# Performance work log

Hardware: AMD Instinct MI355X
Metric: run time of the kernel (lower is better)

Reference implementation:

```python
import jax, jax.numpy as jnp
import numpy as np

KE = 14.3996
ALPHA = 0.3
CUTOFF = 10.0
K_MAX = 6
N_ATOMS = 100000
N_PAIRS = 6400000
N_MOL = 64


def _generate_kvecs():
    kr = np.arange(0, K_MAX + 1, dtype=np.float32)
    kr = np.concatenate([kr, -kr[1:]])
    # cartesian product of (kr, kr, kr)
    g = np.stack(np.meshgrid(kr, kr, kr, indexing='ij'), axis=-1).reshape(-1, 3)
    norm = (g ** 2).sum(axis=1)
    mask = (norm <= K_MAX ** 2 + 2) & (norm != 0)
    return jnp.asarray(g[mask])  # [1020, 3]


def setup_inputs() -> dict:
    key = jax.random.key(0)
    k1, k2, k3, k4, k5, k6, k7 = jax.random.split(key, 7)
    partial_charges = jax.random.normal(k1, (N_ATOMS, 1), dtype=jnp.float32)
    # pair displacement vectors; scale so typical |r_ij| ~ 3-6 A, avoids d ~ 0
    Rij = jax.random.normal(k2, (N_PAIRS, 3), dtype=jnp.float32) * 3.0 + 1.0
    R = jax.random.uniform(k3, (N_ATOMS, 3), dtype=jnp.float32) * 20.0
    # orthorhombic-ish invertible cells: diag(~20) + small perturbation
    cell = jnp.eye(3, dtype=jnp.float32)[None] * 20.0 \
        + jax.random.uniform(k4, (N_MOL, 3, 3), dtype=jnp.float32) * 0.1
    idx_m = jnp.sort(jax.random.randint(k5, (N_ATOMS,), 0, N_MOL)).astype(jnp.int64)
    idx_i = jax.random.randint(k6, (N_PAIRS,), 0, N_ATOMS).astype(jnp.int64)
    idx_j = jax.random.randint(k7, (N_PAIRS,), 0, N_ATOMS).astype(jnp.int64)
    kvecs = _generate_kvecs()
    return {"partial_charges": partial_charges, "Rij": Rij, "R": R, "cell": cell,
            "kvecs": kvecs, "idx_m": idx_m, "idx_i": idx_i, "idx_j": idx_j}


def reference(partial_charges, Rij, R, cell, kvecs, idx_m, idx_i, idx_j):
    q = partial_charges.squeeze(-1)                      # [A]
    d_ij = jnp.linalg.norm(Rij, axis=1)                  # [P]
    sqrt_a = jnp.sqrt(jnp.float32(ALPHA))

    # ---- real space: gather q, erfc-screened pair potential, double scatter ----
    f_r = jax.scipy.special.erfc(sqrt_a * d_ij) / d_ij
    f_r_cut = jax.scipy.special.erfc(sqrt_a * CUTOFF) / CUTOFF
    pot_ij = q[idx_i] * q[idx_j] * (f_r - f_r_cut)
    pot_ij = jnp.where(d_ij <= CUTOFF, pot_ij, jnp.zeros_like(pot_ij))
    y_atom = jax.ops.segment_sum(pot_ij, idx_i, num_segments=N_ATOMS)
    y_real = 0.5 * KE * jax.ops.segment_sum(y_atom, idx_m, num_segments=N_MOL)

    # ---- reciprocal space ----
    two_pi = 2.0 * jnp.float32(np.pi)
    recip_box = two_pi * jnp.transpose(jnp.linalg.inv(cell), (0, 2, 1))  # [M,3,3]
    v_box = jnp.abs(jnp.linalg.det(cell))                                # [M]
    prefactor = two_pi / v_box
    kv = jnp.einsum('kd,mde->mke', kvecs, recip_box)     # [M,K,3]
    k_sq = jnp.sum(kv ** 2, axis=2)                      # [M,K]
    q_gauss = jnp.exp(-0.25 * k_sq / ALPHA)              # [M,K]
    # per-atom phase: gather per-molecule k-vectors, dot with positions
    kdp = jnp.einsum('akd,ad->ak', kv[idx_m], R)         # [A,K]
    q_real = jax.ops.segment_sum(q[:, None] * jnp.cos(kdp), idx_m, num_segments=N_MOL)
    q_imag = jax.ops.segment_sum(q[:, None] * jnp.sin(kdp), idx_m, num_segments=N_MOL)
    q_dens = q_real ** 2 + q_imag ** 2                   # [M,K]
    y_ewald = prefactor * jnp.sum(q_dens * q_gauss / k_sq, axis=1)
    self_int = jnp.sqrt(ALPHA / np.pi) * jax.ops.segment_sum(q ** 2, idx_m, num_segments=N_MOL)
    y_recip = KE * (y_ewald - self_int)

    return y_real + y_recip                              # [M]
```

## Files before the change

kernel.cpp:

```cpp
#include <hip/hip_runtime.h>
#include <math.h>

#define KE_C     14.3996f
#define ALPHA_C  0.3f
#define CUTOFF_C 10.0f
#define TWO_PI_C 6.283185307179586f
#define ASPL     32
#define NK2      512
#define NREAL    2048

typedef float vfloat4 __attribute__((ext_vector_type(4)));
typedef int   vint4   __attribute__((ext_vector_type(4)));

__device__ __forceinline__ void sincos_rev(float x, float* s, float* c) {
    float f = __builtin_amdgcn_fractf(x);
    *s = __builtin_amdgcn_sinf(f);
    *c = __builtin_amdgcn_cosf(f);
}

__device__ __forceinline__ float inv3x3(const float* c, float* inv) {
    float a00 = c[0], a01 = c[1], a02 = c[2];
    float a10 = c[3], a11 = c[4], a12 = c[5];
    float a20 = c[6], a21 = c[7], a22 = c[8];
    float det = a00 * (a11 * a22 - a12 * a21)
              - a01 * (a10 * a22 - a12 * a20)
              + a02 * (a10 * a21 - a11 * a20);
    float id = 1.0f / det;
    inv[0] = (a11 * a22 - a12 * a21) * id;
    inv[1] = (a02 * a21 - a01 * a22) * id;
    inv[2] = (a01 * a12 - a02 * a11) * id;
    inv[3] = (a12 * a20 - a10 * a22) * id;
    inv[4] = (a00 * a22 - a02 * a20) * id;
    inv[5] = (a02 * a10 - a00 * a12) * id;
    inv[6] = (a10 * a21 - a11 * a20) * id;
    inv[7] = (a01 * a20 - a00 * a21) * id;
    inv[8] = (a00 * a11 - a01 * a10) * id;
    return det;
}

__global__ __launch_bounds__(256) void k_setup(const float* __restrict__ R,
                                               const float* __restrict__ q,
                                               const int* __restrict__ idx_m,
                                               const float* __restrict__ cell,
                                               const float* __restrict__ kvecs,
                                               float4* __restrict__ S4,
                                               float2* __restrict__ QM,
                                               float* __restrict__ SI,
                                               int* __restrict__ bounds,
                                               float4* __restrict__ KH,
                                               int* __restrict__ cnt,
                                               int natoms, int nmol, int nk, int NA) {
    int bid = blockIdx.x;
    int tid = threadIdx.x;
    if (bid < NA) {
        __shared__ float si[64];
        if (tid < 64) si[tid] = 0.0f;
        __syncthreads();
        int a = bid * 256 + tid;
        if (a < natoms) {
            int m = idx_m[a];
            float inv[9];
            inv3x3(cell + m * 9, inv);
            float r0 = R[3 * a], r1 = R[3 * a + 1], r2 = R[3 * a + 2];
            float s0 = inv[0] * r0 + inv[3] * r1 + inv[6] * r2;
            float s1 = inv[1] * r0 + inv[4] * r1 + inv[7] * r2;
            float s2 = inv[2] * r0 + inv[5] * r1 + inv[8] * r2;
            float qa = q[a];
            S4[a] = make_float4(s0, s1, s2, qa);
            QM[a] = make_float2(qa, __int_as_float(m));
            atomicAdd(&si[m & 63], qa * qa);
        }
        __syncthreads();
        if (tid < 64) atomicAdd(&SI[tid], si[tid]);
    } else if (bid == NA) {
        int m = tid;
        if (m <= nmol) {
            int lo = 0, hi = natoms;
            while (lo < hi) {
                int mid = (lo + hi) >> 1;
                if (idx_m[mid] < m) lo = mid + 1; else hi = mid;
            }
            bounds[m] = lo;
        }
    } else {
        for (int k = tid; k < nk; k += 256) {
            float gx = kvecs[3 * k], gy = kvecs[3 * k + 1], gz = kvecs[3 * k + 2];
            bool pos = (gx > 0.5f) ||
                       (fabsf(gx) < 0.5f && (gy > 0.5f ||
                        (fabsf(gy) < 0.5f && gz > 0.5f)));
            if (pos) {
                int s = atomicAdd(cnt, 1);
                KH[s] = make_float4(gx, gy, gz, 0.0f);
            }
        }
    }
}

__global__ __launch_bounds__(256) void k_recip(const float4* __restrict__ S4,
                                               const float4* __restrict__ KH,
                                               const int* __restrict__ bounds,
                                               float* __restrict__ QR,
                                               float* __restrict__ QI) {
    int tid = threadIdx.x;
    int bid = blockIdx.x;
    int m  = bid / ASPL;
    int ac = bid % ASPL;
    int s0 = bounds[m], s1 = bounds[m + 1];
    int per = (s1 - s0 + ASPL - 1) / ASPL;
    int a0 = s0 + ac * per;
    int a1 = min(a0 + per, s1);
    float4 g0 = KH[tid];
    float4 g1 = KH[tid + 256];
    float qr0 = 0.f, qi0 = 0.f, qr1 = 0.f, qi1 = 0.f;
#pragma unroll 4
    for (int t = a0; t < a1; ++t) {
        float4 s = S4[t];
        float ph0 = fmaf(g0.x, s.x, fmaf(g0.y, s.y, g0.z * s.z));
        float ph1 = fmaf(g1.x, s.x, fmaf(g1.y, s.y, g1.z * s.z));
        float sn0, cs0, sn1, cs1;
        sincos_rev(ph0, &sn0, &cs0);
        sincos_rev(ph1, &sn1, &cs1);
        qr0 = fmaf(s.w, cs0, qr0);
        qi0 = fmaf(s.w, sn0, qi0);
        qr1 = fmaf(s.w, cs1, qr1);
        qi1 = fmaf(s.w, sn1, qi1);
    }
    atomicAdd(&QR[m * NK2 + tid], qr0);
    atomicAdd(&QI[m * NK2 + tid], qi0);
    atomicAdd(&QR[m * NK2 + tid + 256], qr1);
    atomicAdd(&QI[m * NK2 + tid + 256], qi1);
}

__global__ __launch_bounds__(256, 8) void k_real(const float* __restrict__ Rij,
                                                 const int* __restrict__ idx_i,
                                                 const int* __restrict__ idx_j,
                                                 const float2* __restrict__ QM,
                                                 float* __restrict__ YRpad, int npairs) {
    __shared__ float acc[4][64];
    int tid = threadIdx.x;
    int wave = tid >> 6;
    acc[wave][tid & 63] = 0.0f;
    __syncthreads();
    const float sqa = 0.5477225575051661f;
    const float frcut = erfcf(sqa * CUTOFF_C) / CUTOFF_C;
    int nchunk = npairs >> 2;
    int stride = NREAL * 256;
    for (int c = blockIdx.x * 256 + tid; c < nchunk; c += stride) {
        int p = c << 2;
        vint4 ii = *(const vint4*)(idx_i + p);
        vint4 jj = *(const vint4*)(idx_j + p);
        const vfloat4* r4 = (const vfloat4*)(Rij + 3 * p);
        vfloat4 ra = r4[0], rb = r4[1], rc = r4[2];
        float x0 = ra.x, y0 = ra.y, z0 = ra.z;
        float x1 = ra.w, y1 = rb.x, z1 = rb.y;
        float x2 = rb.z, y2 = rb.w, z2 = rc.x;
        float x3 = rc.y, y3 = rc.z, z3 = rc.w;
        float2 qi0 = QM[ii.x], qi1 = QM[ii.y], qi2 = QM[ii.z], qi3 = QM[ii.w];
        float2 qj0 = QM[jj.x], qj1 = QM[jj.y], qj2 = QM[jj.z], qj3 = QM[jj.w];
        float d0 = sqrtf(x0 * x0 + y0 * y0 + z0 * z0);
        float d1 = sqrtf(x1 * x1 + y1 * y1 + z1 * z1);
        float d2 = sqrtf(x2 * x2 + y2 * y2 + z2 * z2);
        float d3 = sqrtf(x3 * x3 + y3 * y3 + z3 * z3);
        if (d0 <= CUTOFF_C)
            atomicAdd(&acc[wave][__float_as_int(qi0.y) & 63],
                      qi0.x * qj0.x * (erfcf(sqa * d0) / d0 - frcut));
        if (d1 <= CUTOFF_C)
            atomicAdd(&acc[wave][__float_as_int(qi1.y) & 63],
                      qi1.x * qj1.x * (erfcf(sqa * d1) / d1 - frcut));
        if (d2 <= CUTOFF_C)
            atomicAdd(&acc[wave][__float_as_int(qi2.y) & 63],
                      qi2.x * qj2.x * (erfcf(sqa * d2) / d2 - frcut));
        if (d3 <= CUTOFF_C)
            atomicAdd(&acc[wave][__float_as_int(qi3.y) & 63],
                      qi3.x * qj3.x * (erfcf(sqa * d3) / d3 - frcut));
    }
    if (blockIdx.x == 0 && tid == 0) {
        for (int p = (npairs >> 2) << 2; p < npairs; ++p) {
            float x = Rij[3 * p], y = Rij[3 * p + 1], z = Rij[3 * p + 2];
            float d = sqrtf(x * x + y * y + z * z);
            if (d <= CUTOFF_C) {
                float2 qi = QM[idx_i[p]];
                float2 qj = QM[idx_j[p]];
                atomicAdd(&acc[0][__float_as_int(qi.y) & 63],
                          qi.x * qj.x * (erfcf(sqa * d) / d - frcut));
            }
        }
    }
    __syncthreads();
    if (tid < 64) {
        float v = acc[0][tid] + acc[1][tid] + acc[2][tid] + acc[3][tid];
        atomicAdd(&YRpad[tid * 16], v);
    }
}

__global__ __launch_bounds__(256) void k_final(const float4* __restrict__ KH,
                                               const int* __restrict__ cnt,
                                               const float* __restrict__ cell,
                                               const float* __restrict__ QR,
                                               const float* __restrict__ QI,
                                               const float* __restrict__ YRpad,
                                               const float* __restrict__ SI,
                                               float* __restrict__ out) {
    int m = blockIdx.x;
    int tid = threadIdx.x;
    __shared__ float wsum[4];
    float inv[9];
    float det = inv3x3(cell + m * 9, inv);
    int nhalf = cnt[0];
    float acc = 0.0f;
    for (int k = tid; k < nhalf; k += 256) {
        float4 g = KH[k];
        float kv0 = TWO_PI_C * (g.x * inv[0] + g.y * inv[1] + g.z * inv[2]);
        float kv1 = TWO_PI_C * (g.x * inv[3] + g.y * inv[4] + g.z * inv[5]);
        float kv2 = TWO_PI_C * (g.x * inv[6] + g.y * inv[7] + g.z * inv[8]);
        float ksq = kv0 * kv0 + kv1 * kv1 + kv2 * kv2;
        float qr = QR[m * NK2 + k], qi = QI[m * NK2 + k];
        acc += (qr * qr + qi * qi) * __expf(-0.25f / ALPHA_C * ksq) / ksq;
    }
#pragma unroll
    for (int off = 32; off > 0; off >>= 1) acc += __shfl_down(acc, off, 64);
    if ((tid & 63) == 0) wsum[tid >> 6] = acc;
    __syncthreads();
    if (tid == 0) {
        float s = 2.0f * (wsum[0] + wsum[1] + wsum[2] + wsum[3]);
        float pref = TWO_PI_C / fabsf(det);
        float self_c = sqrtf(ALPHA_C / 3.14159265358979323846f);
        out[m] = 0.5f * KE_C * YRpad[m * 16] + KE_C * (pref * s - self_c * SI[m]);
    }
}

extern "C" void kernel_launch(void* const* d_in, const int* in_sizes, int n_in,
                              void* d_out, int out_size, void* d_ws, size_t ws_size,
                              hipStream_t stream) {
    const float* q     = (const float*)d_in[0];
    const float* Rij   = (const float*)d_in[1];
    const float* R     = (const float*)d_in[2];
    const float* cell  = (const float*)d_in[3];
    const float* kvecs = (const float*)d_in[4];
    const int*   idx_m = (const int*)d_in[5];
    const int*   idx_i = (const int*)d_in[6];
    const int*   idx_j = (const int*)d_in[7];

    int natoms = in_sizes[0];
    int npairs = in_sizes[1] / 3;
    int nmol   = in_sizes[3] / 9;
    int nk     = in_sizes[4] / 3;
    float* out = (float*)d_out;

    float*  W      = (float*)d_ws;
    int*    bounds = (int*)W;
    float4* S4     = (float4*)(W + 80);
    float2* QM     = (float2*)(W + 80 + 4 * (size_t)natoms);
    size_t  zoff   = 80 + 6 * (size_t)natoms;
    zoff = (zoff + 3) & ~(size_t)3;
    float4* KH     = (float4*)(W + zoff);
    float*  QR     = W + zoff + 4 * NK2;
    float*  QI     = QR + (size_t)nmol * NK2;
    float*  SI     = QI + (size_t)nmol * NK2;
    float*  YRpad  = SI + 64;
    int*    cnt    = (int*)(YRpad + 64 * 16);
    size_t zero_bytes = (4 * NK2 + (size_t)2 * nmol * NK2 + 64 + 64 * 16 + 4) * sizeof(float);
    (void)hipMemsetAsync(KH, 0, zero_bytes, stream);

    int NA = (natoms + 255) / 256;
    k_setup<<<NA + 2, 256, 0, stream>>>(R, q, idx_m, cell, kvecs, S4, QM, SI,
                                        bounds, KH, cnt, natoms, nmol, nk, NA);
    k_recip<<<nmol * ASPL, 256, 0, stream>>>(S4, KH, bounds, QR, QI);
    k_real <<<NREAL, 256, 0, stream>>>(Rij, idx_i, idx_j, QM, YRpad, npairs);
    k_final<<<nmol, 256, 0, stream>>>(KH, cnt, cell, QR, QI, YRpad, SI, out);
}
```

Measured before the change: 240.6 us.

## Bin real-space pairs by atom blocks so charge gathers hit LDS

Replaces the single real-space pair kernel with two passes. The first pass computes the screened pair potential, groups pairs into buckets keyed by the 4096-atom blocks of i and j, and writes compact (value, packed local indices) records. The second pass loads both blocks' charges into shared memory and accumulates the per-molecule sums from there. Charge and molecule id are packed into one word by stealing low mantissa bits, which costs a little precision. The change also adds extra global write and read traffic, a fixed per-bucket capacity that silently drops pairs on overflow, and a dependency on workspace size to enable the path.

```diff
diff --git a/kernel.cpp b/kernel.cpp
--- a/kernel.cpp
+++ b/kernel.cpp
@@ -8,6 +8,14 @@
 #define ASPL     32
 #define NK2      512
 #define NREAL    2048
+
+#define SHB      12
+#define NSL      25
+#define NBKT     (NSL * NSL)
+#define CAP      11264
+#define PA_BLOCKS 1024
+#define PA_TILE   1024
+#define CCHUNK    2
 
 typedef float vfloat4 __attribute__((ext_vector_type(4)));
 typedef int   vint4   __attribute__((ext_vector_type(4)));
@@ -45,6 +53,7 @@
                                                const float* __restrict__ kvecs,
                                                float4* __restrict__ S4,
                                                float2* __restrict__ QM,
+                                               unsigned int* __restrict__ QP,
                                                float* __restrict__ SI,
                                                int* __restrict__ bounds,
                                                float4* __restrict__ KH,
@@ -68,6 +77,7 @@
             float qa = q[a];
             S4[a] = make_float4(s0, s1, s2, qa);
             QM[a] = make_float2(qa, __int_as_float(m));
+            QP[a] = (__float_as_uint(qa) & ~63u) | (unsigned int)(m & 63);
             atomicAdd(&si[m & 63], qa * qa);
         }
         __syncthreads();
@@ -129,6 +139,116 @@
     atomicAdd(&QI[m * NK2 + tid], qi0);
     atomicAdd(&QR[m * NK2 + tid + 256], qr1);
     atomicAdd(&QI[m * NK2 + tid + 256], qi1);
+}
+
+__global__ __launch_bounds__(256) void k_binA(const float* __restrict__ Rij,
+                                              const int* __restrict__ idx_i,
+                                              const int* __restrict__ idx_j,
+                                              float2* __restrict__ Bkt,
+                                              int* __restrict__ gcnt, int npairs) {
+    __shared__ int h[NBKT];
+    __shared__ int pos[NBKT];
+    int tid = threadIdx.x;
+    const float sqa = 0.5477225575051661f;
+    const float frcut = erfcf(sqa * CUTOFF_C) / CUTOFF_C;
+    for (int base = blockIdx.x * PA_TILE; base < npairs; base += PA_BLOCKS * PA_TILE) {
+        for (int t = tid; t < NBKT; t += 256) h[t] = 0;
+        __syncthreads();
+        int p = base + tid * 4;
+        float fk[4];
+        int bk[4] = {-1, -1, -1, -1};
+        unsigned int pkk[4];
+#define DOPAIR(k, xx, yy, zz, iv, jv)                                         \
+        {                                                                     \
+            float d2_ = fmaf(xx, xx, fmaf(yy, yy, (zz) * (zz)));              \
+            float d_ = sqrtf(d2_);                                            \
+            if (d_ <= CUTOFF_C) {                                             \
+                fk[k] = erfcf(sqa * d_) / d_ - frcut;                         \
+                bk[k] = ((iv) >> SHB) * NSL + ((jv) >> SHB);                  \
+                pkk[k] = (unsigned int)(((iv) & 4095) | (((jv) & 4095) << SHB)); \
+            }                                                                 \
+        }
+        if (p + 4 <= npairs) {
+            vint4 ii = *(const vint4*)(idx_i + p);
+            vint4 jj = *(const vint4*)(idx_j + p);
+            const vfloat4* r4 = (const vfloat4*)(Rij + 3 * p);
+            vfloat4 ra = r4[0], rb = r4[1], rc = r4[2];
+            DOPAIR(0, ra.x, ra.y, ra.z, ii.x, jj.x)
+            DOPAIR(1, ra.w, rb.x, rb.y, ii.y, jj.y)
+            DOPAIR(2, rb.z, rb.w, rc.x, ii.z, jj.z)
+            DOPAIR(3, rc.y, rc.z, rc.w, ii.w, jj.w)
+        } else {
+#pragma unroll
+            for (int k = 0; k < 4; ++k) {
+                int pp = p + k;
+                if (pp < npairs) {
+                    float x = Rij[3 * pp], y = Rij[3 * pp + 1], z = Rij[3 * pp + 2];
+                    int iv = idx_i[pp], jv = idx_j[pp];
+                    DOPAIR(k, x, y, z, iv, jv)
+                }
+            }
+        }
+#undef DOPAIR
+#pragma unroll
+        for (int k = 0; k < 4; ++k)
+            if (bk[k] >= 0) atomicAdd(&h[bk[k]], 1);
+        __syncthreads();
+        for (int t = tid; t < NBKT; t += 256) {
+            int c = h[t];
+            pos[t] = c ? atomicAdd(&gcnt[t], c) : 0;
+        }
+        __syncthreads();
+#pragma unroll
+        for (int k = 0; k < 4; ++k)
+            if (bk[k] >= 0) {
+                int g = atomicAdd(&pos[bk[k]], 1);
+                if (g < CAP)
+                    Bkt[(size_t)bk[k] * CAP + g] = make_float2(fk[k], __uint_as_float(pkk[k]));
+            }
+        __syncthreads();
+    }
+}
+
+__global__ __launch_bounds__(256) void k_binB(const float2* __restrict__ Bkt,
+                                              const int* __restrict__ gcnt,
+                                              const unsigned int* __restrict__ QP,
+                                              float* __restrict__ YRpad, int natoms) {
+    __shared__ unsigned int Qi[4096];
+    __shared__ unsigned int Qj[4096];
+    __shared__ float acc[4][64];
+    int tid = threadIdx.x;
+    int wave = tid >> 6;
+    int b = blockIdx.x / CCHUNK;
+    int part = blockIdx.x % CCHUNK;
+    int si = b / NSL, sj = b % NSL;
+    int bi = si << SHB, bj = sj << SHB;
+    for (int t = tid; t < 4096; t += 256) {
+        int ai = bi + t;
+        Qi[t] = (ai < natoms) ? QP[ai] : 0u;
+        int aj = bj + t;
+        Qj[t] = (aj < natoms) ? QP[aj] : 0u;
+    }
+    acc[wave][tid & 63] = 0.0f;
+    __syncthreads();
+    int n = min(gcnt[b], CAP);
+    int lo = (n * part) / CCHUNK;
+    int hi = (n * (part + 1)) / CCHUNK;
+    const float2* src = Bkt + (size_t)b * CAP;
+    for (int r = lo + tid; r < hi; r += 256) {
+        float2 rec = src[r];
+        unsigned int pk = __float_as_uint(rec.y);
+        unsigned int il = pk & 4095u;
+        unsigned int jl = (pk >> SHB) & 4095u;
+        unsigned int up = Qi[il];
+        float qi = __uint_as_float(up & ~63u);
+        float qj = __uint_as_float(Qj[jl] & ~63u);
+        atomicAdd(&acc[wave][up & 63u], qi * qj * rec.x);
+    }
+    __syncthreads();
+    if (tid < 64) {
+        float v = acc[0][tid] + acc[1][tid] + acc[2][tid] + acc[3][tid];
+        if (v != 0.0f) atomicAdd(&YRpad[tid * 16], v);
+    }
 }
 
 __global__ __launch_bounds__(256, 8) void k_real(const float* __restrict__ Rij,
@@ -251,7 +371,8 @@
     int*    bounds = (int*)W;
     float4* S4     = (float4*)(W + 80);
     float2* QM     = (float2*)(W + 80 + 4 * (size_t)natoms);
-    size_t  zoff   = 80 + 6 * (size_t)natoms;
+    unsigned int* QP = (unsigned int*)(W + 80 + 6 * (size_t)natoms);
+    size_t  zoff   = 80 + 7 * (size_t)natoms;
     zoff = (zoff + 3) & ~(size_t)3;
     float4* KH     = (float4*)(W + zoff);
     float*  QR     = W + zoff + 4 * NK2;
@@ -259,13 +380,26 @@
     float*  SI     = QI + (size_t)nmol * NK2;
     float*  YRpad  = SI + 64;
     int*    cnt    = (int*)(YRpad + 64 * 16);
-    size_t zero_bytes = (4 * NK2 + (size_t)2 * nmol * NK2 + 64 + 64 * 16 + 4) * sizeof(float);
+    int*    gcnt   = cnt + 4;
+    size_t  boff   = (size_t)(gcnt + NBKT - (int*)W);
+    boff = (boff + 3) & ~(size_t)3;
+    float2* Bkt    = (float2*)(W + boff);
+    size_t  need   = (boff + 2 * (size_t)NBKT * CAP) * sizeof(float);
+    bool use_bin = (ws_size >= need);
+
+    size_t zero_bytes = (4 * NK2 + (size_t)2 * nmol * NK2 + 64 + 64 * 16 + 4 + NBKT) * sizeof(float);
     (void)hipMemsetAsync(KH, 0, zero_bytes, stream);
 
     int NA = (natoms + 255) / 256;
-    k_setup<<<NA + 2, 256, 0, stream>>>(R, q, idx_m, cell, kvecs, S4, QM, SI,
+    k_setup<<<NA + 2, 256, 0, stream>>>(R, q, idx_m, cell, kvecs, S4, QM, QP, SI,
                                         bounds, KH, cnt, natoms, nmol, nk, NA);
-    k_recip<<<nmol * ASPL, 256, 0, stream>>>(S4, KH, bounds, QR, QI);
-    k_real <<<NREAL, 256, 0, stream>>>(Rij, idx_i, idx_j, QM, YRpad, npairs);
+    if (use_bin) {
+        k_binA<<<PA_BLOCKS, 256, 0, stream>>>(Rij, idx_i, idx_j, Bkt, gcnt, npairs);
+        k_recip<<<nmol * ASPL, 256, 0, stream>>>(S4, KH, bounds, QR, QI);
+        k_binB<<<NBKT * CCHUNK, 256, 0, stream>>>(Bkt, gcnt, QP, YRpad, natoms);
+    } else {
+        k_recip<<<nmol * ASPL, 256, 0, stream>>>(S4, KH, bounds, QR, QI);
+        k_real<<<NREAL, 256, 0, stream>>>(Rij, idx_i, idx_j, QM, YRpad, npairs);
+    }
     k_final<<<nmol, 256, 0, stream>>>(KH, cnt, cell, QR, QI, YRpad, SI, out);
 }
```

Result: slower. 422.2 us (+75.5%).

## Fuse reciprocal and real-space kernels; replace memset with in-kernel zeroing and partials

Applied to the files above, without the earlier changes.

Merges the reciprocal-space structure-factor pass into the real-space pair kernel, so the first 256 blocks do a per-molecule k-sum (4 blocks per molecule instead of 32) before joining the grid-stride pair loop. The host memset goes away: accumulators are zeroed inside the setup kernel. Self-interaction sums become per-block partials written without atomics and reduced in the final kernel. This saves a launch and a memset and lets the two phases overlap, but the 256 recip blocks now carry far more sincos work and may become stragglers that delay the real-space work.

```diff
diff --git a/kernel.cpp b/kernel.cpp
--- a/kernel.cpp
+++ b/kernel.cpp
@@ -5,9 +5,10 @@
 #define ALPHA_C  0.3f
 #define CUTOFF_C 10.0f
 #define TWO_PI_C 6.283185307179586f
-#define ASPL     32
 #define NK2      512
+#define NRB      256
 #define NREAL    2048
+#define NAP      400
 
 typedef float vfloat4 __attribute__((ext_vector_type(4)));
 typedef int   vint4   __attribute__((ext_vector_type(4)));
@@ -45,10 +46,13 @@
                                                const float* __restrict__ kvecs,
                                                float4* __restrict__ S4,
                                                float2* __restrict__ QM,
-                                               float* __restrict__ SI,
+                                               float* __restrict__ SIpart,
                                                int* __restrict__ bounds,
                                                float4* __restrict__ KH,
                                                int* __restrict__ cnt,
+                                               float* __restrict__ QR,
+                                               float* __restrict__ QI,
+                                               float* __restrict__ YRpad,
                                                int natoms, int nmol, int nk, int NA) {
     int bid = blockIdx.x;
     int tid = threadIdx.x;
@@ -71,7 +75,7 @@
             atomicAdd(&si[m & 63], qa * qa);
         }
         __syncthreads();
-        if (tid < 64) atomicAdd(&SI[tid], si[tid]);
+        if (tid < 64) SIpart[(size_t)tid * NAP + bid] = si[tid];
     } else if (bid == NA) {
         int m = tid;
         if (m <= nmol) {
@@ -82,7 +86,9 @@
             }
             bounds[m] = lo;
         }
-    } else {
+    } else if (bid == NA + 1) {
+        if (tid == 0) *cnt = 0;
+        __syncthreads();
         for (int k = tid; k < nk; k += 256) {
             float gx = kvecs[3 * k], gy = kvecs[3 * k + 1], gz = kvecs[3 * k + 2];
             bool pos = (gx > 0.5f) ||
@@ -93,59 +99,71 @@
                 KH[s] = make_float4(gx, gy, gz, 0.0f);
             }
         }
-    }
-}
-
-__global__ __launch_bounds__(256) void k_recip(const float4* __restrict__ S4,
-                                               const float4* __restrict__ KH,
-                                               const int* __restrict__ bounds,
-                                               float* __restrict__ QR,
-                                               float* __restrict__ QI) {
-    int tid = threadIdx.x;
-    int bid = blockIdx.x;
-    int m  = bid / ASPL;
-    int ac = bid % ASPL;
-    int s0 = bounds[m], s1 = bounds[m + 1];
-    int per = (s1 - s0 + ASPL - 1) / ASPL;
-    int a0 = s0 + ac * per;
-    int a1 = min(a0 + per, s1);
-    float4 g0 = KH[tid];
-    float4 g1 = KH[tid + 256];
-    float qr0 = 0.f, qi0 = 0.f, qr1 = 0.f, qi1 = 0.f;
-#pragma unroll 4
-    for (int t = a0; t < a1; ++t) {
-        float4 s = S4[t];
-        float ph0 = fmaf(g0.x, s.x, fmaf(g0.y, s.y, g0.z * s.z));
-        float ph1 = fmaf(g1.x, s.x, fmaf(g1.y, s.y, g1.z * s.z));
-        float sn0, cs0, sn1, cs1;
-        sincos_rev(ph0, &sn0, &cs0);
-        sincos_rev(ph1, &sn1, &cs1);
-        qr0 = fmaf(s.w, cs0, qr0);
-        qi0 = fmaf(s.w, sn0, qi0);
-        qr1 = fmaf(s.w, cs1, qr1);
-        qi1 = fmaf(s.w, sn1, qi1);
-    }
-    atomicAdd(&QR[m * NK2 + tid], qr0);
-    atomicAdd(&QI[m * NK2 + tid], qi0);
-    atomicAdd(&QR[m * NK2 + tid + 256], qr1);
-    atomicAdd(&QI[m * NK2 + tid + 256], qi1);
-}
-
-__global__ __launch_bounds__(256, 8) void k_real(const float* __restrict__ Rij,
+        __syncthreads();
+        int n = __hip_atomic_load(cnt, __ATOMIC_RELAXED, __HIP_MEMORY_SCOPE_AGENT);
+        for (int s = n + tid; s < NK2; s += 256)
+            KH[s] = make_float4(0.f, 0.f, 0.f, 0.f);
+    } else {
+        int zb = bid - (NA + 2);
+        for (int t = tid; t < NK2; t += 256) {
+            QR[zb * NK2 + t] = 0.0f;
+            QI[zb * NK2 + t] = 0.0f;
+        }
+        if (zb == 0) for (int t = tid; t < 64 * 16; t += 256) YRpad[t] = 0.0f;
+    }
+}
+
+__global__ __launch_bounds__(256, 8) void k_mega(const float4* __restrict__ S4,
+                                                 const float4* __restrict__ KH,
+                                                 const int* __restrict__ bounds,
+                                                 float* __restrict__ QR,
+                                                 float* __restrict__ QI,
+                                                 const float* __restrict__ Rij,
                                                  const int* __restrict__ idx_i,
                                                  const int* __restrict__ idx_j,
                                                  const float2* __restrict__ QM,
                                                  float* __restrict__ YRpad, int npairs) {
     __shared__ float acc[4][64];
     int tid = threadIdx.x;
+    int bid = blockIdx.x;
     int wave = tid >> 6;
+
+    if (bid < NRB) {
+        int m  = bid >> 2;
+        int ac = bid & 3;
+        int s0 = bounds[m], s1 = bounds[m + 1];
+        int per = (s1 - s0 + 3) >> 2;
+        int a0 = s0 + ac * per;
+        int a1 = min(a0 + per, s1);
+        float4 g0 = KH[tid];
+        float4 g1 = KH[tid + 256];
+        float qr0 = 0.f, qi0 = 0.f, qr1 = 0.f, qi1 = 0.f;
+#pragma unroll 4
+        for (int t = a0; t < a1; ++t) {
+            float4 s = S4[t];
+            float ph0 = fmaf(g0.x, s.x, fmaf(g0.y, s.y, g0.z * s.z));
+            float ph1 = fmaf(g1.x, s.x, fmaf(g1.y, s.y, g1.z * s.z));
+            float sn0, cs0, sn1, cs1;
+            sincos_rev(ph0, &sn0, &cs0);
+            sincos_rev(ph1, &sn1, &cs1);
+            qr0 = fmaf(s.w, cs0, qr0);
+            qi0 = fmaf(s.w, sn0, qi0);
+            qr1 = fmaf(s.w, cs1, qr1);
+            qi1 = fmaf(s.w, sn1, qi1);
+        }
+        atomicAdd(&QR[m * NK2 + tid], qr0);
+        atomicAdd(&QI[m * NK2 + tid], qi0);
+        atomicAdd(&QR[m * NK2 + tid + 256], qr1);
+        atomicAdd(&QI[m * NK2 + tid + 256], qi1);
+    }
+
     acc[wave][tid & 63] = 0.0f;
     __syncthreads();
     const float sqa = 0.5477225575051661f;
     const float frcut = erfcf(sqa * CUTOFF_C) / CUTOFF_C;
     int nchunk = npairs >> 2;
     int stride = NREAL * 256;
-    for (int c = blockIdx.x * 256 + tid; c < nchunk; c += stride) {
+    for (int c = bid * 256 + tid; c < nchunk; c += stride) {
         int p = c << 2;
         vint4 ii = *(const vint4*)(idx_i + p);
         vint4 jj = *(const vint4*)(idx_j + p);
@@ -174,7 +192,7 @@
             atomicAdd(&acc[wave][__float_as_int(qi3.y) & 63],
                       qi3.x * qj3.x * (erfcf(sqa * d3) / d3 - frcut));
     }
-    if (blockIdx.x == 0 && tid == 0) {
+    if (bid == 0 && tid == 0) {
         for (int p = (npairs >> 2) << 2; p < npairs; ++p) {
             float x = Rij[3 * p], y = Rij[3 * p + 1], z = Rij[3 * p + 2];
             float d = sqrtf(x * x + y * y + z * z);
@@ -199,15 +217,15 @@
                                                const float* __restrict__ QR,
                                                const float* __restrict__ QI,
                                                const float* __restrict__ YRpad,
-                                               const float* __restrict__ SI,
-                                               float* __restrict__ out) {
+                                               const float* __restrict__ SIpart,
+                                               float* __restrict__ out, int NA) {
     int m = blockIdx.x;
     int tid = threadIdx.x;
-    __shared__ float wsum[4];
+    __shared__ float wsum[4], wsi[4];
     float inv[9];
     float det = inv3x3(cell + m * 9, inv);
     int nhalf = cnt[0];
-    float acc = 0.0f;
+    float acc = 0.0f, si = 0.0f;
     for (int k = tid; k < nhalf; k += 256) {
         float4 g = KH[k];
         float kv0 = TWO_PI_C * (g.x * inv[0] + g.y * inv[1] + g.z * inv[2]);
@@ -217,15 +235,20 @@
         float qr = QR[m * NK2 + k], qi = QI[m * NK2 + k];
         acc += (qr * qr + qi * qi) * __expf(-0.25f / ALPHA_C * ksq) / ksq;
     }
+    for (int b = tid; b < NA; b += 256) si += SIpart[(size_t)m * NAP + b];
 #pragma unroll
-    for (int off = 32; off > 0; off >>= 1) acc += __shfl_down(acc, off, 64);
-    if ((tid & 63) == 0) wsum[tid >> 6] = acc;
+    for (int off = 32; off > 0; off >>= 1) {
+        acc += __shfl_down(acc, off, 64);
+        si  += __shfl_down(si,  off, 64);
+    }
+    if ((tid & 63) == 0) { wsum[tid >> 6] = acc; wsi[tid >> 6] = si; }
     __syncthreads();
     if (tid == 0) {
-        float s = 2.0f * (wsum[0] + wsum[1] + wsum[2] + wsum[3]);
+        float s  = 2.0f * (wsum[0] + wsum[1] + wsum[2] + wsum[3]);
+        float st = wsi[0] + wsi[1] + wsi[2] + wsi[3];
         float pref = TWO_PI_C / fabsf(det);
         float self_c = sqrtf(ALPHA_C / 3.14159265358979323846f);
-        out[m] = 0.5f * KE_C * YRpad[m * 16] + KE_C * (pref * s - self_c * SI[m]);
+        out[m] = 0.5f * KE_C * YRpad[m * 16] + KE_C * (pref * s - self_c * st);
     }
 }
 
@@ -251,21 +274,20 @@
     int*    bounds = (int*)W;
     float4* S4     = (float4*)(W + 80);
     float2* QM     = (float2*)(W + 80 + 4 * (size_t)natoms);
-    size_t  zoff   = 80 + 6 * (size_t)natoms;
-    zoff = (zoff + 3) & ~(size_t)3;
-    float4* KH     = (float4*)(W + zoff);
-    float*  QR     = W + zoff + 4 * NK2;
+    size_t  off    = 80 + 6 * (size_t)natoms;
+    off = (off + 3) & ~(size_t)3;
+    float4* KH     = (float4*)(W + off);
+    float*  QR     = W + off + 4 * NK2;
     float*  QI     = QR + (size_t)nmol * NK2;
-    float*  SI     = QI + (size_t)nmol * NK2;
-    float*  YRpad  = SI + 64;
-    int*    cnt    = (int*)(YRpad + 64 * 16);
-    size_t zero_bytes = (4 * NK2 + (size_t)2 * nmol * NK2 + 64 + 64 * 16 + 4) * sizeof(float);
-    (void)hipMemsetAsync(KH, 0, zero_bytes, stream);
+    float*  YRpad  = QI + (size_t)nmol * NK2;
+    float*  SIpart = YRpad + 64 * 16;
+    int*    cnt    = (int*)(SIpart + 64 * NAP);
 
     int NA = (natoms + 255) / 256;
-    k_setup<<<NA + 2, 256, 0, stream>>>(R, q, idx_m, cell, kvecs, S4, QM, SI,
-                                        bounds, KH, cnt, natoms, nmol, nk, NA);
-    k_recip<<<nmol * ASPL, 256, 0, stream>>>(S4, KH, bounds, QR, QI);
-    k_real <<<NREAL, 256, 0, stream>>>(Rij, idx_i, idx_j, QM, YRpad, npairs);
-    k_final<<<nmol, 256, 0, stream>>>(KH, cnt, cell, QR, QI, YRpad, SI, out);
-}
+    k_setup<<<NA + 2 + 64, 256, 0, stream>>>(R, q, idx_m, cell, kvecs, S4, QM,
+                                             SIpart, bounds, KH, cnt, QR, QI,
+                                             YRpad, natoms, nmol, nk, NA);
+    k_mega <<<NREAL, 256, 0, stream>>>(S4, KH, bounds, QR, QI,
+                                       Rij, idx_i, idx_j, QM, YRpad, npairs);
+    k_final<<<nmol, 256, 0, stream>>>(KH, cnt, cell, QR, QI, YRpad, SIpart, out, NA);
+}
```

Measured after the change: 218.7 us (median of 2 runs). -9.1%, faster.
